# Optimization experiments

Hardware: AMD Instinct MI355X
Metric: run time of the kernel (lower is better)

The kernel has to match this reference:

```python
import jax, jax.numpy as jnp
import numpy as np

EMBED = 1024
HEADS = 16
HEAD_DIM = EMBED // HEADS


def setup_inputs() -> dict:
    key = jax.random.key(0)
    ks = jax.random.split(key, 8)
    N, S, E = 4, 2048, EMBED
    s = 1.0 / np.sqrt(E)
    return {
        "values": jax.random.normal(ks[0], (N, S, E), jnp.float32),
        "keys": jax.random.normal(ks[1], (N, S, E), jnp.float32),
        "queries": jax.random.normal(ks[2], (N, S, E), jnp.float32),
        # nn.Linear weights stored as (out_features, in_features)
        "Wv": jax.random.normal(ks[3], (E, E), jnp.float32) * s,
        "Wk": jax.random.normal(ks[4], (E, E), jnp.float32) * s,
        "Wq": jax.random.normal(ks[5], (E, E), jnp.float32) * s,
        "Wo": jax.random.normal(ks[6], (E, E), jnp.float32) * s,
        "bo": jax.random.normal(ks[7], (E,), jnp.float32) * s,
    }


def reference(values, keys, queries, Wv, Wk, Wq, Wo, bo):
    N = queries.shape[0]
    H, D, E = HEADS, HEAD_DIM, EMBED
    # projections (torch Linear: x @ W.T), reshape to [N, S, H, D]
    v = (values @ Wv.T).reshape(N, -1, H, D)
    k = (keys @ Wk.T).reshape(N, -1, H, D)
    q = (queries @ Wq.T).reshape(N, -1, H, D)
    energy = jnp.einsum("nqhd,nkhd->nhqk", q, k)
    # NOTE: original scales by sqrt(embed_size), not sqrt(head_dim)
    attn = jax.nn.softmax(energy / jnp.sqrt(jnp.float32(E)), axis=3)
    out = jnp.einsum("nhql,nlhd->nqhd", attn, v).reshape(N, -1, H * D)
    return out @ Wo.T + bo
```

## Files before the change

### kernel.cpp

```cpp
#include <hip/hip_runtime.h>

typedef __bf16  bf16x8 __attribute__((ext_vector_type(8)));
typedef float   f32x4  __attribute__((ext_vector_type(4)));
typedef unsigned short u16x8 __attribute__((ext_vector_type(8)));

__device__ __forceinline__ unsigned short f2bf(float f) {
    union { float f; unsigned int u; } v; v.f = f;
    unsigned int u = v.u;
    unsigned int r = (u + 0x7fffu + ((u >> 16) & 1u)) >> 16;
    return (unsigned short)r;
}

__device__ __forceinline__ unsigned int pkbf(float lo, float hi) {
    union { float f; unsigned int u; } a, b; a.f = lo; b.f = hi;
    return __builtin_amdgcn_perm(b.u + 0x8000u, a.u + 0x8000u, 0x07060302u);
}

__device__ __forceinline__ void gld_lds16(const unsigned short* g, unsigned short* l) {
    auto gp = (const __attribute__((address_space(1))) unsigned int*)(const void*)g;
    auto lp = (__attribute__((address_space(3))) unsigned int*)(unsigned int)(unsigned long long)(void*)l;
    __builtin_amdgcn_global_load_lds(gp, lp, 16, 0, 0);
}

__global__ void cast4_kernel(const float* __restrict__ a, const float* __restrict__ b,
                             const float* __restrict__ c, const float* __restrict__ d,
                             unsigned short* __restrict__ dst) {
    int sel = blockIdx.x >> 10;
    int off4 = (blockIdx.x & 1023) * 256 + threadIdx.x;
    const float* src = sel == 0 ? a : sel == 1 ? b : sel == 2 ? c : d;
    float4 f = ((const float4*)src)[off4];
    uint2 pk; pk.x = pkbf(f.x, f.y); pk.y = pkbf(f.z, f.w);
    ((uint2*)(dst + (size_t)sel * 1048576))[off4] = pk;
}

__global__ void cast_kernel(const float* __restrict__ src, unsigned short* __restrict__ dst, int n4) {
    int stride = gridDim.x * 256;
    for (int i = blockIdx.x * 256 + threadIdx.x; i < n4; i += stride) {
        float4 f = ((const float4*)src)[i];
        uint2 pk; pk.x = pkbf(f.x, f.y); pk.y = pkbf(f.z, f.w);
        ((uint2*)dst)[i] = pk;
    }
}

template <int MODE>
__global__ __launch_bounds__(256, 3)
void gemm_bt(const unsigned short* __restrict__ A, const unsigned short* __restrict__ Bt,
             void* __restrict__ dst, const float* __restrict__ bias, float a_scale)
{
    constexpr int K = 1024;
    __shared__ unsigned short As[2][4096];
    __shared__ unsigned short Bs[2][4096];

    const int t    = threadIdx.x;
    const int lane = t & 63;
    const int w    = t >> 6;
    const int q    = lane >> 4;
    const int ln   = lane & 15;
    const int wr   = w >> 1, wc = w & 1;
    const int m0   = blockIdx.x * 128;
    const int n0   = blockIdx.y * 128;
    const int srow = lane >> 2;
    const int scol = (lane & 3) * 8;

    f32x4 acc[4][4];
    const f32x4 zz = {0.f, 0.f, 0.f, 0.f};
#pragma unroll
    for (int i = 0; i < 4; ++i)
#pragma unroll
        for (int j = 0; j < 4; ++j) acc[i][j] = zz;

    auto stage = [&](int k0, int p) {
#pragma unroll
        for (int c = 0; c < 2; ++c) {
            int u = w * 2 + c;
            gld_lds16(A  + (size_t)(m0 + u * 16 + srow) * K + k0 + scol, &As[p][u * 512]);
            gld_lds16(Bt + (size_t)(n0 + u * 16 + srow) * K + k0 + scol, &Bs[p][u * 512]);
        }
    };

    stage(0, 0);
    for (int j = 0; j < 32; ++j) {
        __syncthreads();
        if (j < 31) stage((j + 1) * 32, (j + 1) & 1);
        const int p = j & 1;
        bf16x8 af[4], bfr[4];
#pragma unroll
        for (int i = 0; i < 4; ++i)
            af[i] = *(const bf16x8*)&As[p][(wr * 64 + i * 16 + ln) * 32 + q * 8];
#pragma unroll
        for (int jj = 0; jj < 4; ++jj)
            bfr[jj] = *(const bf16x8*)&Bs[p][(wc * 64 + jj * 16 + ln) * 32 + q * 8];
#pragma unroll
        for (int i = 0; i < 4; ++i)
#pragma unroll
            for (int jj = 0; jj < 4; ++jj)
                acc[i][jj] = __builtin_amdgcn_mfma_f32_16x16x32_bf16(af[i], bfr[jj], acc[i][jj], 0, 0, 0);
    }

#pragma unroll
    for (int i = 0; i < 4; ++i) {
#pragma unroll
        for (int j = 0; j < 4; ++j) {
            f32x4 c = acc[i][j];
            int mb = m0 + wr * 64 + i * 16 + q * 4;
            int nn = n0 + wc * 64 + j * 16 + ln;
            if constexpr (MODE == 1) {
                int b = mb >> 11, s = mb & 2047, h = nn >> 6, d = nn & 63;
                uint2 pk;
                pk.x = pkbf(c[0], c[1]);
                pk.y = pkbf(c[2], c[3]);
                size_t idx = (((size_t)(b * 16 + h) * 64) + d) * 2048 + s;
                *(uint2*)&((unsigned short*)dst)[idx] = pk;
            } else {
#pragma unroll
                for (int r = 0; r < 4; ++r) {
                    int m = mb + r;
                    float val = c[r] * a_scale;
                    if constexpr (MODE == 2) {
                        ((float*)dst)[(size_t)m * 1024 + nn] = val + bias[nn];
                    } else {
                        int b = m >> 11, s = m & 2047, h = nn >> 6, d = nn & 63;
                        size_t idx = (((size_t)(b * 16 + h) * 2048) + s) * 64 + d;
                        ((unsigned short*)dst)[idx] = f2bf(val);
                    }
                }
            }
        }
    }
}

__global__ __launch_bounds__(256, 3)
void attn_kernel(const unsigned short* __restrict__ Q, const unsigned short* __restrict__ Kg,
                 const unsigned short* __restrict__ Vt, unsigned short* __restrict__ Og)
{
    __shared__ unsigned short Ks[2][4096];
    __shared__ unsigned short Vs[2][4096];
    __shared__ unsigned short Ps[128 * 72];

    const int t    = threadIdx.x;
    const int lane = t & 63;
    const int w    = t >> 6;
    const int q    = lane >> 4;
    const int ln   = lane & 15;
    const int head = blockIdx.x;
    const int qt   = blockIdx.y;

    const unsigned short* Qh  = Q  + (size_t)head * 2048 * 64;
    const unsigned short* Kh  = Kg + (size_t)head * 2048 * 64;
    const unsigned short* Vth = Vt + (size_t)head * 64 * 2048;

    const int srow = lane >> 2;
    const int scol = (lane & 3) * 8;

    bf16x8 qf[2][2];
    const int rowb = qt * 128 + w * 32;
#pragma unroll
    for (int ti = 0; ti < 2; ++ti)
#pragma unroll
        for (int kc = 0; kc < 2; ++kc)
            qf[ti][kc] = *(const bf16x8*)&Qh[(size_t)(rowb + ti * 16 + ln) * 64 + kc * 32 + q * 8];

    const f32x4 zz = {0.f, 0.f, 0.f, 0.f};
    f32x4 oa[2][4];
#pragma unroll
    for (int ti = 0; ti < 2; ++ti)
#pragma unroll
        for (int dt = 0; dt < 4; ++dt) oa[ti][dt] = zz;
    float l_s[2] = {0.f, 0.f};

    auto stage = [&](int j, int p) {
#pragma unroll
        for (int c = 0; c < 2; ++c) {
            int u = w * 2 + c;
            int kc = u >> 2, rg = u & 3;
            gld_lds16(Kh + (size_t)(j * 64 + rg * 16 + srow) * 64 + kc * 32 + scol,
                      &Ks[p][kc * 2048 + rg * 512]);
            gld_lds16(Vth + (size_t)(rg * 16 + srow) * 2048 + j * 64 + kc * 32 + scol,
                      &Vs[p][kc * 2048 + rg * 512]);
        }
    };

    stage(0, 0);
    for (int j = 0; j < 32; ++j) {
        __syncthreads();
        if (j < 31) stage(j + 1, (j + 1) & 1);
        const int p = j & 1;

        f32x4 sa[4][2];
#pragma unroll
        for (int kt = 0; kt < 4; ++kt)
#pragma unroll
            for (int ti = 0; ti < 2; ++ti) sa[kt][ti] = zz;
#pragma unroll
        for (int kc = 0; kc < 2; ++kc) {
            bf16x8 ka[4];
#pragma unroll
            for (int kt = 0; kt < 4; ++kt)
                ka[kt] = *(const bf16x8*)&Ks[p][kc * 2048 + (kt * 16 + ln) * 32 + q * 8];
#pragma unroll
            for (int kt = 0; kt < 4; ++kt)
#pragma unroll
                for (int ti = 0; ti < 2; ++ti)
                    sa[kt][ti] = __builtin_amdgcn_mfma_f32_16x16x32_bf16(ka[kt], qf[ti][kc], sa[kt][ti], 0, 0, 0);
        }

#pragma unroll
        for (int ti = 0; ti < 2; ++ti) {
            float rs = 0.f;
            const int prow = w * 32 + ti * 16 + ln;
#pragma unroll
            for (int kt = 0; kt < 4; ++kt) {
                float p0 = exp2f(sa[kt][ti][0]);
                float p1 = exp2f(sa[kt][ti][1]);
                float p2 = exp2f(sa[kt][ti][2]);
                float p3 = exp2f(sa[kt][ti][3]);
                rs += (p0 + p1) + (p2 + p3);
                uint2 pk;
                pk.x = pkbf(p0, p1);
                pk.y = pkbf(p2, p3);
                *(uint2*)&Ps[prow * 72 + kt * 16 + q * 4] = pk;
            }
            rs += __shfl_xor(rs, 16);
            rs += __shfl_xor(rs, 32);
            l_s[ti] += rs;
        }

#pragma unroll
        for (int kc = 0; kc < 2; ++kc) {
            bf16x8 va[4], pb[2];
#pragma unroll
            for (int dt = 0; dt < 4; ++dt)
                va[dt] = *(const bf16x8*)&Vs[p][kc * 2048 + (dt * 16 + ln) * 32 + q * 8];
#pragma unroll
            for (int ti = 0; ti < 2; ++ti)
                pb[ti] = *(const bf16x8*)&Ps[(w * 32 + ti * 16 + ln) * 72 + kc * 32 + q * 8];
#pragma unroll
            for (int ti = 0; ti < 2; ++ti)
#pragma unroll
                for (int dt = 0; dt < 4; ++dt)
                    oa[ti][dt] = __builtin_amdgcn_mfma_f32_16x16x32_bf16(va[dt], pb[ti], oa[ti][dt], 0, 0, 0);
        }
    }

    const int n = head >> 4;
    const int hbase = (head & 15) * 64;
#pragma unroll
    for (int ti = 0; ti < 2; ++ti) {
        float inv = 1.f / l_s[ti];
        int sr = qt * 128 + w * 32 + ti * 16 + ln;
        size_t base = ((size_t)n * 2048 + sr) * 1024 + hbase;
#pragma unroll
        for (int dt = 0; dt < 4; ++dt) {
            uint2 pk;
            pk.x = pkbf(oa[ti][dt][0] * inv, oa[ti][dt][1] * inv);
            pk.y = pkbf(oa[ti][dt][2] * inv, oa[ti][dt][3] * inv);
            *(uint2*)&Og[base + dt * 16 + q * 4] = pk;
        }
    }
}

extern "C" void kernel_launch(void* const* d_in, const int* in_sizes, int n_in,
                              void* d_out, int out_size, void* d_ws, size_t ws_size,
                              hipStream_t stream)
{
    (void)in_sizes; (void)n_in; (void)out_size; (void)ws_size;
    const float* values  = (const float*)d_in[0];
    const float* keys    = (const float*)d_in[1];
    const float* queries = (const float*)d_in[2];
    const float* Wv = (const float*)d_in[3];
    const float* Wk = (const float*)d_in[4];
    const float* Wq = (const float*)d_in[5];
    const float* Wo = (const float*)d_in[6];
    const float* bo = (const float*)d_in[7];
    float* out = (float*)d_out;

    unsigned short* ws   = (unsigned short*)d_ws;
    unsigned short* Wv_b = ws;
    unsigned short* Wk_b = ws + 1048576;
    unsigned short* Wq_b = ws + 2097152;
    unsigned short* Wo_b = ws + 3145728;
    unsigned short* Act  = ws + 4194304;
    unsigned short* Ob   = Act;
    unsigned short* Qb   = ws + 12582912;
    unsigned short* Kb   = Qb + 8388608;
    unsigned short* Vtb  = Kb + 8388608;

    cast4_kernel<<<4096, 256, 0, stream>>>(Wv, Wk, Wq, Wo, ws);

    dim3 g(64, 8), b(256);
    const float qscale = 1.4426950408889634f / 32.f;

    cast_kernel<<<4096, 256, 0, stream>>>(values, Act, 2097152);
    gemm_bt<1><<<g, b, 0, stream>>>(Act, Wv_b, Vtb, nullptr, 1.f);
    cast_kernel<<<4096, 256, 0, stream>>>(keys, Act, 2097152);
    gemm_bt<0><<<g, b, 0, stream>>>(Act, Wk_b, Kb, nullptr, 1.f);
    cast_kernel<<<4096, 256, 0, stream>>>(queries, Act, 2097152);
    gemm_bt<0><<<g, b, 0, stream>>>(Act, Wq_b, Qb, nullptr, qscale);

    attn_kernel<<<dim3(64, 16), b, 0, stream>>>(Qb, Kb, Vtb, Ob);
    gemm_bt<2><<<g, b, 0, stream>>>(Ob, Wo_b, out, bo, 1.f);
}
```

Measured before the change: 373.7 us.

## Fuse activation casts into a batched QKV GEMM, enlarge attention tiles, split-K output

The three separate fp32→bf16 activation casts and three projection GEMMs become one batched QKV GEMM launch. It stages fp32 activations straight into swizzled LDS and converts them to bf16 while loading the fragments, which removes the cast kernels and their extra global round-trips. The attention kernel now gives each block 256 query rows (64 per wave) and computes S one K-tile at a time, so each staged K/V tile is reused across more queries; launch bounds drop to 2 blocks per CU. The output projection uses split-K over two slices with fp32 atomicAdd into a memset output, which adds atomic traffic and a memset in exchange for more parallel blocks.

```diff
diff --git a/kernel.cpp b/kernel.cpp
--- a/kernel.cpp
+++ b/kernel.cpp
@@ -16,9 +16,9 @@
     return __builtin_amdgcn_perm(b.u + 0x8000u, a.u + 0x8000u, 0x07060302u);
 }
 
-__device__ __forceinline__ void gld_lds16(const unsigned short* g, unsigned short* l) {
-    auto gp = (const __attribute__((address_space(1))) unsigned int*)(const void*)g;
-    auto lp = (__attribute__((address_space(3))) unsigned int*)(unsigned int)(unsigned long long)(void*)l;
+__device__ __forceinline__ void gld_lds16(const void* g, void* l) {
+    auto gp = (const __attribute__((address_space(1))) unsigned int*)g;
+    auto lp = (__attribute__((address_space(3))) unsigned int*)(unsigned int)(unsigned long long)l;
     __builtin_amdgcn_global_load_lds(gp, lp, 16, 0, 0);
 }
 
@@ -33,23 +33,30 @@
     ((uint2*)(dst + (size_t)sel * 1048576))[off4] = pk;
 }
 
-__global__ void cast_kernel(const float* __restrict__ src, unsigned short* __restrict__ dst, int n4) {
-    int stride = gridDim.x * 256;
-    for (int i = blockIdx.x * 256 + threadIdx.x; i < n4; i += stride) {
-        float4 f = ((const float4*)src)[i];
-        uint2 pk; pk.x = pkbf(f.x, f.y); pk.y = pkbf(f.z, f.w);
-        ((uint2*)dst)[i] = pk;
-    }
-}
-
-template <int MODE>
+__device__ __forceinline__ bf16x8 read_af32(const float* As, int R, int q) {
+    const int m = R & 7;
+    const float4 v0 = *(const float4*)&As[R * 32 + (((2 * q)     ^ m) * 4)];
+    const float4 v1 = *(const float4*)&As[R * 32 + (((2 * q + 1) ^ m) * 4)];
+    union { unsigned int u[4]; bf16x8 v; } r;
+    r.u[0] = pkbf(v0.x, v0.y); r.u[1] = pkbf(v0.z, v0.w);
+    r.u[2] = pkbf(v1.x, v1.y); r.u[3] = pkbf(v1.z, v1.w);
+    return r.v;
+}
+
 __global__ __launch_bounds__(256, 3)
-void gemm_bt(const unsigned short* __restrict__ A, const unsigned short* __restrict__ Bt,
-             void* __restrict__ dst, const float* __restrict__ bias, float a_scale)
+void qkv_gemm(const float* __restrict__ Vg, const float* __restrict__ Kg,
+              const float* __restrict__ Qg, const unsigned short* __restrict__ W,
+              unsigned short* __restrict__ Vtb, unsigned short* __restrict__ Kb,
+              unsigned short* __restrict__ Qb, float qscale)
 {
     constexpr int K = 1024;
-    __shared__ unsigned short As[2][4096];
-    __shared__ unsigned short Bs[2][4096];
+    __shared__ float          Asf[2][4096];
+    __shared__ unsigned short Bs [2][4096];
+
+    const int z = blockIdx.z;
+    const float* A = z == 0 ? Vg : (z == 1 ? Kg : Qg);
+    const unsigned short* Bt = W + (size_t)z * 1048576;
+    const float a_scale = z == 2 ? qscale : 1.f;
 
     const int t    = threadIdx.x;
     const int lane = t & 63;
@@ -59,8 +66,9 @@
     const int wr   = w >> 1, wc = w & 1;
     const int m0   = blockIdx.x * 128;
     const int n0   = blockIdx.y * 128;
-    const int srow = lane >> 2;
-    const int scol = (lane & 3) * 8;
+    const int srow = lane >> 2, scol = (lane & 3) * 8;
+    const int arow = lane >> 3;
+    const int achk = (lane & 7) ^ (arow & 7);
 
     f32x4 acc[4][4];
     const f32x4 zz = {0.f, 0.f, 0.f, 0.f};
@@ -71,9 +79,12 @@
 
     auto stage = [&](int k0, int p) {
 #pragma unroll
+        for (int s = 0; s < 4; ++s)
+            gld_lds16(A + (size_t)(m0 + w * 32 + s * 8 + arow) * K + k0 + achk * 4,
+                      &Asf[p][w * 1024 + s * 256 + lane * 4]);
+#pragma unroll
         for (int c = 0; c < 2; ++c) {
             int u = w * 2 + c;
-            gld_lds16(A  + (size_t)(m0 + u * 16 + srow) * K + k0 + scol, &As[p][u * 512]);
             gld_lds16(Bt + (size_t)(n0 + u * 16 + srow) * K + k0 + scol, &Bs[p][u * 512]);
         }
     };
@@ -86,7 +97,7 @@
         bf16x8 af[4], bfr[4];
 #pragma unroll
         for (int i = 0; i < 4; ++i)
-            af[i] = *(const bf16x8*)&As[p][(wr * 64 + i * 16 + ln) * 32 + q * 8];
+            af[i] = read_af32(Asf[p], wr * 64 + i * 16 + ln, q);
 #pragma unroll
         for (int jj = 0; jj < 4; ++jj)
             bfr[jj] = *(const bf16x8*)&Bs[p][(wc * 64 + jj * 16 + ln) * 32 + q * 8];
@@ -104,38 +115,102 @@
             f32x4 c = acc[i][j];
             int mb = m0 + wr * 64 + i * 16 + q * 4;
             int nn = n0 + wc * 64 + j * 16 + ln;
-            if constexpr (MODE == 1) {
-                int b = mb >> 11, s = mb & 2047, h = nn >> 6, d = nn & 63;
+            int b = mb >> 11, s = mb & 2047, h = nn >> 6, d = nn & 63;
+            if (z == 0) {
                 uint2 pk;
                 pk.x = pkbf(c[0], c[1]);
                 pk.y = pkbf(c[2], c[3]);
                 size_t idx = (((size_t)(b * 16 + h) * 64) + d) * 2048 + s;
-                *(uint2*)&((unsigned short*)dst)[idx] = pk;
+                *(uint2*)&Vtb[idx] = pk;
             } else {
+                unsigned short* dst = z == 1 ? Kb : Qb;
 #pragma unroll
                 for (int r = 0; r < 4; ++r) {
-                    int m = mb + r;
-                    float val = c[r] * a_scale;
-                    if constexpr (MODE == 2) {
-                        ((float*)dst)[(size_t)m * 1024 + nn] = val + bias[nn];
-                    } else {
-                        int b = m >> 11, s = m & 2047, h = nn >> 6, d = nn & 63;
-                        size_t idx = (((size_t)(b * 16 + h) * 2048) + s) * 64 + d;
-                        ((unsigned short*)dst)[idx] = f2bf(val);
-                    }
+                    size_t idx = (((size_t)(b * 16 + h) * 2048) + (s + r)) * 64 + d;
+                    dst[idx] = f2bf(c[r] * a_scale);
                 }
             }
         }
     }
 }
 
-__global__ __launch_bounds__(256, 3)
+__global__ __launch_bounds__(256, 4)
+void out_gemm(const unsigned short* __restrict__ A, const unsigned short* __restrict__ Bt,
+              float* __restrict__ out, const float* __restrict__ bias)
+{
+    constexpr int K = 1024;
+    __shared__ unsigned short As[2][4096];
+    __shared__ unsigned short Bs[2][4096];
+
+    const int t    = threadIdx.x;
+    const int lane = t & 63;
+    const int w    = t >> 6;
+    const int q    = lane >> 4;
+    const int ln   = lane & 15;
+    const int wr   = w >> 1, wc = w & 1;
+    const int m0   = blockIdx.x * 128;
+    const int n0   = blockIdx.y * 128;
+    const int kb   = blockIdx.z * 512;
+    const int srow = lane >> 2, scol = (lane & 3) * 8;
+
+    f32x4 acc[4][4];
+    const f32x4 zz = {0.f, 0.f, 0.f, 0.f};
+#pragma unroll
+    for (int i = 0; i < 4; ++i)
+#pragma unroll
+        for (int j = 0; j < 4; ++j) acc[i][j] = zz;
+
+    auto stage = [&](int k0, int p) {
+#pragma unroll
+        for (int c = 0; c < 2; ++c) {
+            int u = w * 2 + c;
+            gld_lds16(A  + (size_t)(m0 + u * 16 + srow) * K + k0 + scol, &As[p][u * 512]);
+            gld_lds16(Bt + (size_t)(n0 + u * 16 + srow) * K + k0 + scol, &Bs[p][u * 512]);
+        }
+    };
+
+    stage(kb, 0);
+    for (int j = 0; j < 16; ++j) {
+        __syncthreads();
+        if (j < 15) stage(kb + (j + 1) * 32, (j + 1) & 1);
+        const int p = j & 1;
+        bf16x8 af[4], bfr[4];
+#pragma unroll
+        for (int i = 0; i < 4; ++i)
+            af[i] = *(const bf16x8*)&As[p][(wr * 64 + i * 16 + ln) * 32 + q * 8];
+#pragma unroll
+        for (int jj = 0; jj < 4; ++jj)
+            bfr[jj] = *(const bf16x8*)&Bs[p][(wc * 64 + jj * 16 + ln) * 32 + q * 8];
+#pragma unroll
+        for (int i = 0; i < 4; ++i)
+#pragma unroll
+            for (int jj = 0; jj < 4; ++jj)
+                acc[i][jj] = __builtin_amdgcn_mfma_f32_16x16x32_bf16(af[i], bfr[jj], acc[i][jj], 0, 0, 0);
+    }
+
+    const bool addb = (blockIdx.z == 0);
+#pragma unroll
+    for (int i = 0; i < 4; ++i) {
+#pragma unroll
+        for (int j = 0; j < 4; ++j) {
+            f32x4 c = acc[i][j];
+            int mb = m0 + wr * 64 + i * 16 + q * 4;
+            int nn = n0 + wc * 64 + j * 16 + ln;
+            float bv = addb ? bias[nn] : 0.f;
+#pragma unroll
+            for (int r = 0; r < 4; ++r)
+                atomicAdd(&out[(size_t)(mb + r) * 1024 + nn], c[r] + bv);
+        }
+    }
+}
+
+__global__ __launch_bounds__(256, 2)
 void attn_kernel(const unsigned short* __restrict__ Q, const unsigned short* __restrict__ Kg,
                  const unsigned short* __restrict__ Vt, unsigned short* __restrict__ Og)
 {
     __shared__ unsigned short Ks[2][4096];
     __shared__ unsigned short Vs[2][4096];
-    __shared__ unsigned short Ps[128 * 72];
+    __shared__ unsigned short Ps[256 * 72];
 
     const int t    = threadIdx.x;
     const int lane = t & 63;
@@ -152,31 +227,29 @@
     const int srow = lane >> 2;
     const int scol = (lane & 3) * 8;
 
-    bf16x8 qf[2][2];
-    const int rowb = qt * 128 + w * 32;
-#pragma unroll
-    for (int ti = 0; ti < 2; ++ti)
+    bf16x8 qf[4][2];
+    const int rowb = qt * 256 + w * 64;
+#pragma unroll
+    for (int ti = 0; ti < 4; ++ti)
 #pragma unroll
         for (int kc = 0; kc < 2; ++kc)
             qf[ti][kc] = *(const bf16x8*)&Qh[(size_t)(rowb + ti * 16 + ln) * 64 + kc * 32 + q * 8];
 
     const f32x4 zz = {0.f, 0.f, 0.f, 0.f};
-    f32x4 oa[2][4];
-#pragma unroll
-    for (int ti = 0; ti < 2; ++ti)
+    f32x4 oa[4][4];
+#pragma unroll
+    for (int ti = 0; ti < 4; ++ti)
 #pragma unroll
         for (int dt = 0; dt < 4; ++dt) oa[ti][dt] = zz;
-    float l_s[2] = {0.f, 0.f};
+    float l_s[4] = {0.f, 0.f, 0.f, 0.f};
 
     auto stage = [&](int j, int p) {
 #pragma unroll
-        for (int c = 0; c < 2; ++c) {
-            int u = w * 2 + c;
-            int kc = u >> 2, rg = u & 3;
-            gld_lds16(Kh + (size_t)(j * 64 + rg * 16 + srow) * 64 + kc * 32 + scol,
-                      &Ks[p][kc * 2048 + rg * 512]);
-            gld_lds16(Vth + (size_t)(rg * 16 + srow) * 2048 + j * 64 + kc * 32 + scol,
-                      &Vs[p][kc * 2048 + rg * 512]);
+        for (int kc = 0; kc < 2; ++kc) {
+            gld_lds16(Kh + (size_t)(j * 64 + w * 16 + srow) * 64 + kc * 32 + scol,
+                      &Ks[p][kc * 2048 + w * 512]);
+            gld_lds16(Vth + (size_t)(w * 16 + srow) * 2048 + j * 64 + kc * 32 + scol,
+                      &Vs[p][kc * 2048 + w * 512]);
         }
     };
 
@@ -186,56 +259,49 @@
         if (j < 31) stage(j + 1, (j + 1) & 1);
         const int p = j & 1;
 
-        f32x4 sa[4][2];
-#pragma unroll
-        for (int kt = 0; kt < 4; ++kt)
-#pragma unroll
-            for (int ti = 0; ti < 2; ++ti) sa[kt][ti] = zz;
-#pragma unroll
-        for (int kc = 0; kc < 2; ++kc) {
-            bf16x8 ka[4];
-#pragma unroll
-            for (int kt = 0; kt < 4; ++kt)
-                ka[kt] = *(const bf16x8*)&Ks[p][kc * 2048 + (kt * 16 + ln) * 32 + q * 8];
-#pragma unroll
-            for (int kt = 0; kt < 4; ++kt)
-#pragma unroll
-                for (int ti = 0; ti < 2; ++ti)
-                    sa[kt][ti] = __builtin_amdgcn_mfma_f32_16x16x32_bf16(ka[kt], qf[ti][kc], sa[kt][ti], 0, 0, 0);
-        }
-
-#pragma unroll
-        for (int ti = 0; ti < 2; ++ti) {
-            float rs = 0.f;
-            const int prow = w * 32 + ti * 16 + ln;
-#pragma unroll
-            for (int kt = 0; kt < 4; ++kt) {
-                float p0 = exp2f(sa[kt][ti][0]);
-                float p1 = exp2f(sa[kt][ti][1]);
-                float p2 = exp2f(sa[kt][ti][2]);
-                float p3 = exp2f(sa[kt][ti][3]);
-                rs += (p0 + p1) + (p2 + p3);
+        float rs[4] = {0.f, 0.f, 0.f, 0.f};
+#pragma unroll
+        for (int kt = 0; kt < 4; ++kt) {
+            bf16x8 ka0 = *(const bf16x8*)&Ks[p][(kt * 16 + ln) * 32 + q * 8];
+            bf16x8 ka1 = *(const bf16x8*)&Ks[p][2048 + (kt * 16 + ln) * 32 + q * 8];
+            f32x4 sa[4];
+#pragma unroll
+            for (int ti = 0; ti < 4; ++ti) {
+                sa[ti] = __builtin_amdgcn_mfma_f32_16x16x32_bf16(ka0, qf[ti][0], zz, 0, 0, 0);
+                sa[ti] = __builtin_amdgcn_mfma_f32_16x16x32_bf16(ka1, qf[ti][1], sa[ti], 0, 0, 0);
+            }
+#pragma unroll
+            for (int ti = 0; ti < 4; ++ti) {
+                float p0 = exp2f(sa[ti][0]);
+                float p1 = exp2f(sa[ti][1]);
+                float p2 = exp2f(sa[ti][2]);
+                float p3 = exp2f(sa[ti][3]);
+                rs[ti] += (p0 + p1) + (p2 + p3);
                 uint2 pk;
                 pk.x = pkbf(p0, p1);
                 pk.y = pkbf(p2, p3);
-                *(uint2*)&Ps[prow * 72 + kt * 16 + q * 4] = pk;
+                *(uint2*)&Ps[(w * 64 + ti * 16 + ln) * 72 + kt * 16 + q * 4] = pk;
             }
-            rs += __shfl_xor(rs, 16);
-            rs += __shfl_xor(rs, 32);
-            l_s[ti] += rs;
+        }
+#pragma unroll
+        for (int ti = 0; ti < 4; ++ti) {
+            float r = rs[ti];
+            r += __shfl_xor(r, 16);
+            r += __shfl_xor(r, 32);
+            l_s[ti] += r;
         }
 
 #pragma unroll
         for (int kc = 0; kc < 2; ++kc) {
-            bf16x8 va[4], pb[2];
+            bf16x8 va[4], pb[4];
 #pragma unroll
             for (int dt = 0; dt < 4; ++dt)
                 va[dt] = *(const bf16x8*)&Vs[p][kc * 2048 + (dt * 16 + ln) * 32 + q * 8];
 #pragma unroll
-            for (int ti = 0; ti < 2; ++ti)
-                pb[ti] = *(const bf16x8*)&Ps[(w * 32 + ti * 16 + ln) * 72 + kc * 32 + q * 8];
-#pragma unroll
-            for (int ti = 0; ti < 2; ++ti)
+            for (int ti = 0; ti < 4; ++ti)
+                pb[ti] = *(const bf16x8*)&Ps[(w * 64 + ti * 16 + ln) * 72 + kc * 32 + q * 8];
+#pragma unroll
+            for (int ti = 0; ti < 4; ++ti)
 #pragma unroll
                 for (int dt = 0; dt < 4; ++dt)
                     oa[ti][dt] = __builtin_amdgcn_mfma_f32_16x16x32_bf16(va[dt], pb[ti], oa[ti][dt], 0, 0, 0);
@@ -245,9 +311,9 @@
     const int n = head >> 4;
     const int hbase = (head & 15) * 64;
 #pragma unroll
-    for (int ti = 0; ti < 2; ++ti) {
+    for (int ti = 0; ti < 4; ++ti) {
         float inv = 1.f / l_s[ti];
-        int sr = qt * 128 + w * 32 + ti * 16 + ln;
+        int sr = qt * 256 + w * 64 + ti * 16 + ln;
         size_t base = ((size_t)n * 2048 + sr) * 1024 + hbase;
 #pragma unroll
         for (int dt = 0; dt < 4; ++dt) {
@@ -275,28 +341,20 @@
     float* out = (float*)d_out;
 
     unsigned short* ws   = (unsigned short*)d_ws;
-    unsigned short* Wv_b = ws;
-    unsigned short* Wk_b = ws + 1048576;
-    unsigned short* Wq_b = ws + 2097152;
+    unsigned short* Wb   = ws;
     unsigned short* Wo_b = ws + 3145728;
-    unsigned short* Act  = ws + 4194304;
-    unsigned short* Ob   = Act;
-    unsigned short* Qb   = ws + 12582912;
+    unsigned short* Qb   = ws + 4194304;
     unsigned short* Kb   = Qb + 8388608;
     unsigned short* Vtb  = Kb + 8388608;
-
-    cast4_kernel<<<4096, 256, 0, stream>>>(Wv, Wk, Wq, Wo, ws);
-
-    dim3 g(64, 8), b(256);
+    unsigned short* Ob   = Vtb + 8388608;
+
     const float qscale = 1.4426950408889634f / 32.f;
 
-    cast_kernel<<<4096, 256, 0, stream>>>(values, Act, 2097152);
-    gemm_bt<1><<<g, b, 0, stream>>>(Act, Wv_b, Vtb, nullptr, 1.f);
-    cast_kernel<<<4096, 256, 0, stream>>>(keys, Act, 2097152);
-    gemm_bt<0><<<g, b, 0, stream>>>(Act, Wk_b, Kb, nullptr, 1.f);
-    cast_kernel<<<4096, 256, 0, stream>>>(queries, Act, 2097152);
-    gemm_bt<0><<<g, b, 0, stream>>>(Act, Wq_b, Qb, nullptr, qscale);
-
-    attn_kernel<<<dim3(64, 16), b, 0, stream>>>(Qb, Kb, Vtb, Ob);
-    gemm_bt<2><<<g, b, 0, stream>>>(Ob, Wo_b, out, bo, 1.f);
-}
+    cast4_kernel<<<4096, 256, 0, stream>>>(Wv, Wk, Wq, Wo, Wb);
+    hipMemsetAsync(out, 0, (size_t)8192 * 1024 * 4, stream);
+
+    qkv_gemm<<<dim3(64, 8, 3), 256, 0, stream>>>(values, keys, queries, Wb,
+                                                 Vtb, Kb, Qb, qscale);
+    attn_kernel<<<dim3(64, 8), 256, 0, stream>>>(Qb, Kb, Vtb, Ob);
+    out_gemm<<<dim3(64, 8, 2), 256, 0, stream>>>(Ob, Wo_b, out, bo);
+}
```

Result: slower. 411.6 us (+10.2%).
